# Optimization experiments

Hardware: AMD Instinct MI355X
Metric: run time of the kernel (lower is better)

## Reference

```python
import jax, jax.numpy as jnp
import numpy as np

DIM = 1024
N_HEADS = 16
HEAD_DIM = DIM // N_HEADS


def setup_inputs() -> dict:
    key = jax.random.key(0)
    ks = jax.random.split(key, 7)
    s = 1.0 / np.sqrt(DIM)
    return {
        "hidden_states": jax.random.normal(ks[0], (1, 4096, DIM), dtype=jnp.float32),
        "Wq": jax.random.uniform(ks[1], (DIM, DIM), jnp.float32, -s, s),
        "bq": jax.random.uniform(ks[2], (DIM,), jnp.float32, -s, s),
        "Wk": jax.random.uniform(ks[3], (DIM, DIM), jnp.float32, -s, s),
        "bk": jax.random.uniform(ks[4], (DIM,), jnp.float32, -s, s),
        "Wv": jax.random.uniform(ks[5], (DIM, DIM), jnp.float32, -s, s),
        "bv": jax.random.uniform(ks[6], (DIM,), jnp.float32, -s, s),
    }


def _split_heads(x):
    # [B, S, DIM] -> [B, H, S, HEAD_DIM]
    b, s, _ = x.shape
    return x.reshape(b, s, N_HEADS, HEAD_DIM).transpose(0, 2, 1, 3)


def reference(hidden_states, Wq, bq, Wk, bk, Wv, bv):
    q = _split_heads(hidden_states @ Wq + bq)
    k = _split_heads(hidden_states @ Wk + bk)
    v = _split_heads(hidden_states @ Wv + bv)
    scores = jnp.einsum("bhqd,bhkd->bhqk", q, k) / np.sqrt(HEAD_DIM).astype(np.float32)
    probs = jax.nn.softmax(scores, axis=-1)  # dropout prob = 0 -> identity
    ctx = jnp.einsum("bhqk,bhkd->bhqd", probs, v)
    b, h, s, d = ctx.shape
    return ctx.transpose(0, 2, 1, 3).reshape(b, s, h * d)
```

## Files before the change

### kernel.cpp

```cpp
#include <hip/hip_runtime.h>
#include <hip/hip_bf16.h>

#define S_LEN 4096
#define DIM   1024
#define NH    16
#define HD    64

typedef unsigned short u16;
typedef short  bf16x8 __attribute__((ext_vector_type(8)));
typedef float  f32x4  __attribute__((ext_vector_type(4)));

__device__ __forceinline__ u16 f2bf(float f){
  union { float f; unsigned u; } x; x.f = f;
  unsigned u = x.u;
  return (u16)((u + 0x7FFFu + ((u >> 16) & 1u)) >> 16);
}
__device__ __forceinline__ unsigned pk2(float a, float b){
  union { __hip_bfloat162 h; unsigned u; } x;
  x.h = __float22bfloat162_rn(float2{a, b});
  return x.u;
}
__device__ __forceinline__ void ld2lds16(const u16* g, u16* l){
  __builtin_amdgcn_global_load_lds((const __attribute__((address_space(1))) void*)g,
                                   (__attribute__((address_space(3))) void*)l, 16, 0, 0);
}

#define QSCALE 0.1803368801111204f

__global__ __launch_bounds__(256) void fill_sentinel(float* __restrict__ out, int n){
  int i = blockIdx.x * 256 + threadIdx.x;
  if (i < n) out[i] = 77.0f;
}

__global__ __launch_bounds__(256) void conv_x(const float* __restrict__ X, u16* __restrict__ Xb){
  size_t i = ((size_t)blockIdx.x * 256 + threadIdx.x) * 8;
  float4 v0 = *(const float4*)(X + i);
  float4 v1 = *(const float4*)(X + i + 4);
  uint4 w;
  w.x = pk2(v0.x, v0.y); w.y = pk2(v0.z, v0.w);
  w.z = pk2(v1.x, v1.y); w.w = pk2(v1.z, v1.w);
  *(uint4*)(Xb + i) = w;
}

__global__ __launch_bounds__(256) void transpose_w(
    const float* __restrict__ W0, const float* __restrict__ W1, const float* __restrict__ W2,
    u16* __restrict__ Wt)
{
  const float* W = blockIdx.z==0 ? W0 : blockIdx.z==1 ? W1 : W2;
  u16* T = Wt + (size_t)blockIdx.z * DIM * DIM;
  __shared__ __align__(16) u16 tile[64*72];
  int k0 = blockIdx.x*64, n0 = blockIdx.y*64;
  int t = threadIdx.x;
  #pragma unroll
  for (int i = 0; i < 4; ++i){
    int idx = t + i*256;
    int row = idx >> 4, col4 = (idx & 15) * 4;
    float4 v = *(const float4*)(W + (size_t)(k0+row)*DIM + n0 + col4);
    tile[(col4+0)*72 + row] = f2bf(v.x);
    tile[(col4+1)*72 + row] = f2bf(v.y);
    tile[(col4+2)*72 + row] = f2bf(v.z);
    tile[(col4+3)*72 + row] = f2bf(v.w);
  }
  __syncthreads();
  #pragma unroll
  for (int i = 0; i < 2; ++i){
    int idx = t + i*256;
    int n = idx >> 3, k16 = (idx & 7) * 8;
    *(int4*)(T + (size_t)(n0+n)*DIM + k0 + k16) = *(const int4*)(tile + n*72 + k16);
  }
}

__device__ __forceinline__ void qkv_epilogue(
    int z, int m0, int n0, int wm, int wn, int quad, int l15,
    const f32x4 acc[4][4], const float* bias,
    u16* __restrict__ qb, u16* __restrict__ kf_out, u16* __restrict__ vf_out)
{
  #pragma unroll
  for (int nt=0; nt<4; ++nt){
    int n = n0 + wn + nt*16 + l15;
    float bv = bias[n];
    int h = n >> 6, d = n & 63;
    #pragma unroll
    for (int mt=0; mt<4; ++mt){
      int mb = m0 + wm + mt*16 + quad*4;
      f32x4 c = acc[mt][nt];
      if (z == 0){
        #pragma unroll
        for (int r=0; r<4; ++r)
          qb[(size_t)(mb + r)*DIM + n] = f2bf((c[r] + bv) * QSCALE);
      } else if (z == 1){
        int half = d >> 5, quadk = (d >> 3) & 3, j = d & 7;
        #pragma unroll
        for (int r=0; r<4; ++r){
          int s = mb + r;
          size_t idx = ((((size_t)h*256 + (s >> 4))*2 + half)*64 + quadk*16 + (s & 15))*8 + j;
          kf_out[idx] = f2bf(c[r] + bv);
        }
      } else {
        int kt64 = mb >> 6, c2 = (mb >> 5) & 1, quadv = (mb >> 3) & 3, j0 = mb & 7;
        int dt = d >> 4, l15v = d & 15;
        size_t base = (((((size_t)h*64 + kt64)*4 + dt)*2 + c2)*64 + quadv*16 + l15v)*8 + j0;
        ushort4 p;
        p.x = f2bf(c[0]+bv); p.y = f2bf(c[1]+bv);
        p.z = f2bf(c[2]+bv); p.w = f2bf(c[3]+bv);
        *(ushort4*)(vf_out + base) = p;
      }
    }
  }
}

__global__ __launch_bounds__(256) void qkv_gemm_fast(
    const u16* __restrict__ Xbf, const u16* __restrict__ Wt,
    const float* __restrict__ b0, const float* __restrict__ b1, const float* __restrict__ b2,
    u16* __restrict__ qb, u16* __restrict__ kf_out, u16* __restrict__ vf_out)
{
  int z = blockIdx.z;
  const u16* Wz = Wt + (size_t)z * DIM * DIM;
  const float* bias = z==0 ? b0 : z==1 ? b1 : b2;

  __shared__ __align__(16) u16 As[128*32];
  __shared__ __align__(16) u16 Bs[128*32];

  int m0 = blockIdx.x * 128, n0 = blockIdx.y * 128;
  int t = threadIdx.x, wave = t >> 6, lane = t & 63, quad = lane >> 4, l15 = lane & 15;
  int wm = (wave >> 1) * 64, wn = (wave & 1) * 64;

  f32x4 acc[4][4];
  #pragma unroll
  for (int i=0;i<4;++i)
    #pragma unroll
    for (int j=0;j<4;++j) acc[i][j] = (f32x4){0.f,0.f,0.f,0.f};

  int srow = wave*32 + (lane >> 2);
  int skc  = (lane & 3) * 8;
  const u16* gA0 = Xbf + (size_t)(m0 + srow)*DIM + skc;
  const u16* gA1 = gA0 + (size_t)16*DIM;
  const u16* gB0 = Wz  + (size_t)(n0 + srow)*DIM + skc;
  const u16* gB1 = gB0 + (size_t)16*DIM;
  u16* lA0 = As + srow*32 + skc;
  u16* lA1 = lA0 + 16*32;
  u16* lB0 = Bs + srow*32 + skc;
  u16* lB1 = lB0 + 16*32;

  for (int kt = 0; kt < 32; ++kt){
    int ko = kt * 32;
    __syncthreads();
    ld2lds16(gA0 + ko, lA0);
    ld2lds16(gA1 + ko, lA1);
    ld2lds16(gB0 + ko, lB0);
    ld2lds16(gB1 + ko, lB1);
    __syncthreads();
    bf16x8 af[4], bfr[4];
    #pragma unroll
    for (int mt=0; mt<4; ++mt) af[mt]  = *(const bf16x8*)(As + (wm + mt*16 + l15)*32 + quad*8);
    #pragma unroll
    for (int nt=0; nt<4; ++nt) bfr[nt] = *(const bf16x8*)(Bs + (wn + nt*16 + l15)*32 + quad*8);
    #pragma unroll
    for (int mt=0; mt<4; ++mt)
      #pragma unroll
      for (int nt=0; nt<4; ++nt)
        acc[mt][nt] = __builtin_amdgcn_mfma_f32_16x16x32_bf16(af[mt], bfr[nt], acc[mt][nt], 0, 0, 0);
  }
  qkv_epilogue(z, m0, n0, wm, wn, quad, l15, acc, bias, qb, kf_out, vf_out);
}

__global__ __launch_bounds__(256) void qkv_gemm_legacy(
    const float* __restrict__ X,
    const float* __restrict__ Wq, const float* __restrict__ Wk, const float* __restrict__ Wv,
    const float* __restrict__ b0, const float* __restrict__ b1, const float* __restrict__ b2,
    u16* __restrict__ qb, u16* __restrict__ kf_out, u16* __restrict__ vf_out)
{
  int z = blockIdx.z;
  const float* W    = z==0 ? Wq : z==1 ? Wk : Wv;
  const float* bias = z==0 ? b0 : z==1 ? b1 : b2;

  __shared__ __align__(16) u16 As[128*40];
  __shared__ __align__(16) u16 Bs[128*40];

  int m0 = blockIdx.x * 128, n0 = blockIdx.y * 128;
  int t = threadIdx.x, wave = t >> 6, lane = t & 63, quad = lane >> 4, l15 = lane & 15;
  int wm = (wave >> 1) * 64, wn = (wave & 1) * 64;

  f32x4 acc[4][4];
  #pragma unroll
  for (int i=0;i<4;++i)
    #pragma unroll
    for (int j=0;j<4;++j) acc[i][j] = (f32x4){0.f,0.f,0.f,0.f};

  int sr = t >> 2, sc = (t & 3) * 8;
  const float* gA0 = X + (size_t)(m0 + sr) * DIM + sc;
  const float* gA1 = X + (size_t)(m0 + 64 + sr) * DIM + sc;
  int br = t >> 3, bc = (t & 7) * 16;
  const float* gW = W + (size_t)br * DIM + n0 + bc;

  for (int kt = 0; kt < 32; ++kt){
    int ko = kt * 32;
    float4 a00 = *(const float4*)(gA0 + ko);
    float4 a01 = *(const float4*)(gA0 + ko + 4);
    float4 a10 = *(const float4*)(gA1 + ko);
    float4 a11 = *(const float4*)(gA1 + ko + 4);
    float4 w0  = *(const float4*)(gW + (size_t)ko*DIM);
    float4 w1  = *(const float4*)(gW + (size_t)ko*DIM + 4);
    float4 w2  = *(const float4*)(gW + (size_t)ko*DIM + 8);
    float4 w3  = *(const float4*)(gW + (size_t)ko*DIM + 12);
    int4 pa0, pa1;
    pa0.x = pk2(a00.x,a00.y); pa0.y = pk2(a00.z,a00.w);
    pa0.z = pk2(a01.x,a01.y); pa0.w = pk2(a01.z,a01.w);
    pa1.x = pk2(a10.x,a10.y); pa1.y = pk2(a10.z,a10.w);
    pa1.z = pk2(a11.x,a11.y); pa1.w = pk2(a11.z,a11.w);
    u16 wb[16];
    wb[0]=f2bf(w0.x); wb[1]=f2bf(w0.y); wb[2]=f2bf(w0.z); wb[3]=f2bf(w0.w);
    wb[4]=f2bf(w1.x); wb[5]=f2bf(w1.y); wb[6]=f2bf(w1.z); wb[7]=f2bf(w1.w);
    wb[8]=f2bf(w2.x); wb[9]=f2bf(w2.y); wb[10]=f2bf(w2.z); wb[11]=f2bf(w2.w);
    wb[12]=f2bf(w3.x); wb[13]=f2bf(w3.y); wb[14]=f2bf(w3.z); wb[15]=f2bf(w3.w);
    __syncthreads();
    *(int4*)(As + sr*40 + sc)      = pa0;
    *(int4*)(As + (64+sr)*40 + sc) = pa1;
    #pragma unroll
    for (int j=0;j<16;++j) Bs[(bc+j)*40 + br] = wb[j];
    __syncthreads();
    bf16x8 af[4], bfr[4];
    #pragma unroll
    for (int mt=0; mt<4; ++mt) af[mt]  = *(const bf16x8*)(As + (wm + mt*16 + l15)*40 + quad*8);
    #pragma unroll
    for (int nt=0; nt<4; ++nt) bfr[nt] = *(const bf16x8*)(Bs + (wn + nt*16 + l15)*40 + quad*8);
    #pragma unroll
    for (int mt=0; mt<4; ++mt)
      #pragma unroll
      for (int nt=0; nt<4; ++nt)
        acc[mt][nt] = __builtin_amdgcn_mfma_f32_16x16x32_bf16(af[mt], bfr[nt], acc[mt][nt], 0, 0, 0);
  }
  qkv_epilogue(z, m0, n0, wm, wn, quad, l15, acc, bias, qb, kf_out, vf_out);
}

#define PSTR 72
#define PQS  (16*PSTR)
__global__ __launch_bounds__(256, 2) void attn(
    const u16* __restrict__ Qb, const u16* __restrict__ Kf,
    const u16* __restrict__ Vf, float* __restrict__ out)
{
  int h = blockIdx.y;
  int t = threadIdx.x, wave = t >> 6, lane = t & 63, quad = lane >> 4, l15 = lane & 15;
  int q0 = blockIdx.x * 128 + wave * 32;

  __shared__ __align__(16) u16 Ps[4*4*PQS];
  u16* Pw = Ps + wave * (4*PQS);

  const u16* Kfh = Kf + (size_t)h * 262144;
  const u16* Vfh = Vf + (size_t)h * 262144;

  bf16x8 qf[2][2];
  #pragma unroll
  for (int qs=0; qs<2; ++qs){
    const u16* Qp = Qb + (size_t)(q0 + qs*16 + l15)*DIM + h*HD;
    qf[qs][0] = *(const bf16x8*)(Qp + quad*8);
    qf[qs][1] = *(const bf16x8*)(Qp + 32 + quad*8);
  }

  f32x4 O[2][4];
  #pragma unroll
  for (int qs=0; qs<2; ++qs)
    #pragma unroll
    for (int dt=0; dt<4; ++dt) O[qs][dt] = (f32x4){0.f,0.f,0.f,0.f};
  float lsum[2] = {0.f, 0.f};

  const u16* kbase = Kfh + (size_t)lane*8;
  const u16* vbase = Vfh + (size_t)lane*8;

#define LOAD_TILE(KDST, VDST, T)                                                 \
  do {                                                                           \
    const u16* kb_ = kbase + (size_t)(T)*4096;                                   \
    _Pragma("unroll")                                                            \
    for (int kn=0; kn<4; ++kn)                                                   \
      _Pragma("unroll")                                                          \
      for (int hf=0; hf<2; ++hf)                                                 \
        KDST[kn][hf] = *(const bf16x8*)(kb_ + (kn*2+hf)*512);                    \
    const u16* vb_ = vbase + (size_t)(T)*4096;                                   \
    _Pragma("unroll")                                                            \
    for (int dt=0; dt<4; ++dt)                                                   \
      _Pragma("unroll")                                                          \
      for (int c2=0; c2<2; ++c2)                                                 \
        VDST[dt][c2] = *(const bf16x8*)(vb_ + (dt*2+c2)*512);                    \
  } while(0)

#define ATTN_COMPUTE(KBUF, VBUF, PPAR)                                           \
  do {                                                                           \
    f32x4 st[2][4];                                                              \
    _Pragma("unroll")                                                            \
    for (int qs=0; qs<2; ++qs)                                                   \
      _Pragma("unroll")                                                          \
      for (int kn=0; kn<4; ++kn){                                                \
        f32x4 zz = (f32x4){0.f,0.f,0.f,0.f};                                     \
        zz = __builtin_amdgcn_mfma_f32_16x16x32_bf16(KBUF[kn][0], qf[qs][0], zz, 0,0,0); \
        zz = __builtin_amdgcn_mfma_f32_16x16x32_bf16(KBUF[kn][1], qf[qs][1], zz, 0,0,0); \
        st[qs][kn] = zz;                                                         \
      }                                                                          \
    _Pragma("unroll")                                                            \
    for (int qs=0; qs<2; ++qs){                                                  \
      float ls = 0.f;                                                            \
      u16* Pq = (PPAR) + qs*PQS;                                                 \
      _Pragma("unroll")                                                          \
      for (int kn=0; kn<4; ++kn){                                                \
        _Pragma("unroll")                                                        \
        for (int r=0; r<4; ++r){                                                 \
          float p = __builtin_amdgcn_exp2f(st[qs][kn][r]);                       \
          st[qs][kn][r] = p; ls += p;                                            \
        }                                                                        \
        uint2 w;                                                                 \
        w.x = pk2(st[qs][kn][0], st[qs][kn][1]);                                 \
        w.y = pk2(st[qs][kn][2], st[qs][kn][3]);                                 \
        *(uint2*)(Pq + l15*PSTR + kn*16 + quad*4) = w;                           \
      }                                                                          \
      lsum[qs] += ls;                                                            \
    }                                                                            \
    __builtin_amdgcn_wave_barrier();                                             \
    _Pragma("unroll")                                                            \
    for (int qs=0; qs<2; ++qs){                                                  \
      const u16* Pq = (PPAR) + qs*PQS;                                           \
      bf16x8 pf0 = *(const bf16x8*)(Pq + l15*PSTR + quad*8);                     \
      bf16x8 pf1 = *(const bf16x8*)(Pq + l15*PSTR + 32 + quad*8);                \
      _Pragma("unroll")                                                          \
      for (int dt=0; dt<4; ++dt){                                                \
        f32x4 o = O[qs][dt];                                                     \
        o = __builtin_amdgcn_mfma_f32_16x16x32_bf16(VBUF[dt][0], pf0, o, 0,0,0); \
        o = __builtin_amdgcn_mfma_f32_16x16x32_bf16(VBUF[dt][1], pf1, o, 0,0,0); \
        O[qs][dt] = o;                                                           \
      }                                                                          \
    }                                                                            \
  } while(0)

  bf16x8 KA[4][2], KB[4][2], VA[4][2], VB[4][2];
  LOAD_TILE(KA, VA, 0);

  for (int kt = 0; kt < 64; kt += 2){
    {
      LOAD_TILE(KB, VB, kt+1);
      ATTN_COMPUTE(KA, VA, Pw);
    }
    {
      LOAD_TILE(KA, VA, (kt+2)&63);
      ATTN_COMPUTE(KB, VB, Pw + 2*PQS);
    }
  }
#undef ATTN_COMPUTE
#undef LOAD_TILE

  #pragma unroll
  for (int qs=0; qs<2; ++qs){
    float l = lsum[qs];
    l += __shfl_xor(l, 16, 64);
    l += __shfl_xor(l, 32, 64);
    float inv = 1.0f / l;
    int query = q0 + qs*16 + l15;
    #pragma unroll
    for (int dt=0; dt<4; ++dt){
      float4 v;
      v.x = O[qs][dt][0]*inv; v.y = O[qs][dt][1]*inv;
      v.z = O[qs][dt][2]*inv; v.w = O[qs][dt][3]*inv;
      *(float4*)(out + (size_t)query*DIM + h*HD + dt*16 + quad*4) = v;
    }
  }
}

extern "C" void kernel_launch(void* const* d_in, const int* in_sizes, int n_in,
                              void* d_out, int out_size, void* d_ws, size_t ws_size,
                              hipStream_t stream)
{
  const float* X  = (const float*)d_in[0];
  const float* Wq = (const float*)d_in[1];
  const float* bq = (const float*)d_in[2];
  const float* Wk = (const float*)d_in[3];
  const float* bk = (const float*)d_in[4];
  const float* Wv = (const float*)d_in[5];
  const float* bv = (const float*)d_in[6];
  float* out = (float*)d_out;
  u16*   ws  = (u16*)d_ws;

  const size_t SD = (size_t)S_LEN * DIM;
  const size_t need_fast = (4*SD + 3*(size_t)DIM*DIM) * sizeof(u16);
  const size_t need_min  = (size_t)24 * 1024 * 1024;

  if (ws_size >= need_fast){
    u16* xbf = ws;
    u16* wt  = xbf + SD;
    u16* qb  = wt + 3*(size_t)DIM*DIM;
    u16* kf  = qb + SD;
    u16* vf  = kf + SD;
    conv_x       <<<dim3((int)(SD/8/256)), 256, 0, stream>>>(X, xbf);
    transpose_w  <<<dim3(16,16,3), 256, 0, stream>>>(Wq, Wk, Wv, wt);
    qkv_gemm_fast<<<dim3(32, 8, 3), 256, 0, stream>>>(xbf, wt, bq, bk, bv, qb, kf, vf);
    attn         <<<dim3(32, 16   ), 256, 0, stream>>>(qb, kf, vf, out);
  } else if (ws_size >= need_min){
    u16* qb = ws;
    u16* kf = qb + SD;
    u16* vf = kf + SD;
    qkv_gemm_legacy<<<dim3(32, 8, 3), 256, 0, stream>>>(X, Wq, Wk, Wv, bq, bk, bv, qb, kf, vf);
    attn           <<<dim3(32, 16   ), 256, 0, stream>>>(qb, kf, vf, out);
  } else {
    fill_sentinel<<<(out_size + 255)/256, 256, 0, stream>>>(out, out_size);
  }
}
```

Measured before the change: 217.9 us.

## Keep softmax probabilities in registers by permuting V layout to match MFMA output

The V tensor written by the QKV GEMM epilogue is permuted so that the key ordering matches the register layout of the QK^T MFMA accumulators. This lets the attention kernel pack the exponentiated scores directly into bf16x8 operands for the PV MFMA, removing the LDS write, wave barrier and LDS read of P. It frees shared memory and LDS traffic, but couples the producer layout tightly to the consumer's fragment mapping.

```diff
diff --git a/kernel.cpp b/kernel.cpp
--- a/kernel.cpp
+++ b/kernel.cpp
@@ -97,9 +97,13 @@
           kf_out[idx] = f2bf(c[r] + bv);
         }
       } else {
-        int kt64 = mb >> 6, c2 = (mb >> 5) & 1, quadv = (mb >> 3) & 3, j0 = mb & 7;
-        int dt = d >> 4, l15v = d & 15;
-        size_t base = (((((size_t)h*64 + kt64)*4 + dt)*2 + c2)*64 + quadv*16 + l15v)*8 + j0;
+        int kt64 = mb >> 6;
+        int kn   = (mb >> 4) & 3;
+        int qsl  = (mb >> 2) & 3;
+        int h2   = kn >> 1;
+        int jj0  = (kn & 1) * 4;
+        int dt = d >> 4, dl = d & 15;
+        size_t base = (((((size_t)h*64 + kt64)*4 + dt)*2 + h2)*64 + qsl*16 + dl)*8 + jj0;
         ushort4 p;
         p.x = f2bf(c[0]+bv); p.y = f2bf(c[1]+bv);
         p.z = f2bf(c[2]+bv); p.w = f2bf(c[3]+bv);
@@ -233,8 +237,6 @@
   qkv_epilogue(z, m0, n0, wm, wn, quad, l15, acc, bias, qb, kf_out, vf_out);
 }
 
-#define PSTR 72
-#define PQS  (16*PSTR)
 __global__ __launch_bounds__(256, 2) void attn(
     const u16* __restrict__ Qb, const u16* __restrict__ Kf,
     const u16* __restrict__ Vf, float* __restrict__ out)
@@ -242,9 +244,6 @@
   int h = blockIdx.y;
   int t = threadIdx.x, wave = t >> 6, lane = t & 63, quad = lane >> 4, l15 = lane & 15;
   int q0 = blockIdx.x * 128 + wave * 32;
-
-  __shared__ __align__(16) u16 Ps[4*4*PQS];
-  u16* Pw = Ps + wave * (4*PQS);
 
   const u16* Kfh = Kf + (size_t)h * 262144;
   const u16* Vfh = Vf + (size_t)h * 262144;
@@ -283,7 +282,7 @@
         VDST[dt][c2] = *(const bf16x8*)(vb_ + (dt*2+c2)*512);                    \
   } while(0)
 
-#define ATTN_COMPUTE(KBUF, VBUF, PPAR)                                           \
+#define ATTN_COMPUTE(KBUF, VBUF)                                                 \
   do {                                                                           \
     f32x4 st[2][4];                                                              \
     _Pragma("unroll")                                                            \
@@ -298,32 +297,28 @@
     _Pragma("unroll")                                                            \
     for (int qs=0; qs<2; ++qs){                                                  \
       float ls = 0.f;                                                            \
-      u16* Pq = (PPAR) + qs*PQS;                                                 \
-      _Pragma("unroll")                                                          \
-      for (int kn=0; kn<4; ++kn){                                                \
+      _Pragma("unroll")                                                          \
+      for (int kn=0; kn<4; ++kn)                                                 \
         _Pragma("unroll")                                                        \
         for (int r=0; r<4; ++r){                                                 \
           float p = __builtin_amdgcn_exp2f(st[qs][kn][r]);                       \
           st[qs][kn][r] = p; ls += p;                                            \
         }                                                                        \
-        uint2 w;                                                                 \
-        w.x = pk2(st[qs][kn][0], st[qs][kn][1]);                                 \
-        w.y = pk2(st[qs][kn][2], st[qs][kn][3]);                                 \
-        *(uint2*)(Pq + l15*PSTR + kn*16 + quad*4) = w;                           \
-      }                                                                          \
       lsum[qs] += ls;                                                            \
-    }                                                                            \
-    __builtin_amdgcn_wave_barrier();                                             \
-    _Pragma("unroll")                                                            \
-    for (int qs=0; qs<2; ++qs){                                                  \
-      const u16* Pq = (PPAR) + qs*PQS;                                           \
-      bf16x8 pf0 = *(const bf16x8*)(Pq + l15*PSTR + quad*8);                     \
-      bf16x8 pf1 = *(const bf16x8*)(Pq + l15*PSTR + 32 + quad*8);                \
+      union { uint4 u; bf16x8 v; } pf0, pf1;                                     \
+      pf0.u.x = pk2(st[qs][0][0], st[qs][0][1]);                                 \
+      pf0.u.y = pk2(st[qs][0][2], st[qs][0][3]);                                 \
+      pf0.u.z = pk2(st[qs][1][0], st[qs][1][1]);                                 \
+      pf0.u.w = pk2(st[qs][1][2], st[qs][1][3]);                                 \
+      pf1.u.x = pk2(st[qs][2][0], st[qs][2][1]);                                 \
+      pf1.u.y = pk2(st[qs][2][2], st[qs][2][3]);                                 \
+      pf1.u.z = pk2(st[qs][3][0], st[qs][3][1]);                                 \
+      pf1.u.w = pk2(st[qs][3][2], st[qs][3][3]);                                 \
       _Pragma("unroll")                                                          \
       for (int dt=0; dt<4; ++dt){                                                \
         f32x4 o = O[qs][dt];                                                     \
-        o = __builtin_amdgcn_mfma_f32_16x16x32_bf16(VBUF[dt][0], pf0, o, 0,0,0); \
-        o = __builtin_amdgcn_mfma_f32_16x16x32_bf16(VBUF[dt][1], pf1, o, 0,0,0); \
+        o = __builtin_amdgcn_mfma_f32_16x16x32_bf16(VBUF[dt][0], pf0.v, o, 0,0,0); \
+        o = __builtin_amdgcn_mfma_f32_16x16x32_bf16(VBUF[dt][1], pf1.v, o, 0,0,0); \
         O[qs][dt] = o;                                                           \
       }                                                                          \
     }                                                                            \
@@ -335,11 +330,11 @@
   for (int kt = 0; kt < 64; kt += 2){
     {
       LOAD_TILE(KB, VB, kt+1);
-      ATTN_COMPUTE(KA, VA, Pw);
+      ATTN_COMPUTE(KA, VA);
     }
     {
       LOAD_TILE(KA, VA, (kt+2)&63);
-      ATTN_COMPUTE(KB, VB, Pw + 2*PQS);
+      ATTN_COMPUTE(KB, VB);
     }
   }
 #undef ATTN_COMPUTE
```

New measurement: 253.3 us. +16.2%, slower.
